# Optimization experiments

Measured on AMD Instinct MI355X. Metric: run time of the kernel, lower is better.

The kernel has to match this reference:

```python
import jax, jax.numpy as jnp
import numpy as np

HEAD_DIM = 128
N_HEADS = 16
N_KV_HEADS = 4
ROPE_BASE = 10000.0
TRAIN_SEQ_LEN = 1024


def _rotary_cos_sin(seq_len, rd, base=ROPE_BASE, train_len=TRAIN_SEQ_LEN):
    # NTK-style base scaling when seq_len exceeds training length (matches Rotary.forward)
    if seq_len > train_len:
        scale = seq_len / train_len
        base = base * scale ** (rd / (rd - 2))
    inv_freq = 1.0 / base ** (np.arange(0, rd, 2, dtype=np.float32) / rd)
    freqs = np.outer(np.arange(seq_len, dtype=np.float32), inv_freq)  # [T, rd/2]
    cos = jnp.asarray(np.cos(freqs))[None, :, None, :]  # [1,T,1,rd/2]
    sin = jnp.asarray(np.sin(freqs))[None, :, None, :]
    return cos, sin


def _apply_rotary(x, cos, sin):
    h = x.shape[-1] // 2
    x1, x2 = x[..., :h], x[..., h:]
    return jnp.concatenate((x1 * cos + x2 * sin, -x1 * sin + x2 * cos), axis=-1)


def _rms_norm(x):
    eps = jnp.finfo(x.dtype).eps
    return x * jax.lax.rsqrt(jnp.mean(x * x, axis=-1, keepdims=True) + eps)


def setup_inputs() -> dict:
    key = jax.random.key(0)
    ks = jax.random.split(key, 6)
    B, T, D = 4, 2048, 2048
    x = jax.random.normal(ks[0], (B, T, D), dtype=jnp.float32)
    q_w = jax.random.normal(ks[1], (D, D), dtype=jnp.float32) * 0.02
    k_w = jax.random.normal(ks[2], (N_KV_HEADS * HEAD_DIM, D), dtype=jnp.float32) * 0.02
    v_w = jax.random.normal(ks[3], (N_KV_HEADS * HEAD_DIM, D), dtype=jnp.float32) * 0.02
    out_w = jax.random.normal(ks[4], (D, D), dtype=jnp.float32) * 0.02
    q_gain = jnp.ones((N_HEADS,), dtype=jnp.float32)
    return {"x": x, "q_w": q_w, "k_w": k_w, "v_w": v_w, "out_w": out_w, "q_gain": q_gain}


def reference(x, q_w, k_w, v_w, out_w, q_gain):
    B, T, D = x.shape
    q = (x @ q_w.T).reshape(B, T, N_HEADS, HEAD_DIM)
    k = (x @ k_w.T).reshape(B, T, N_KV_HEADS, HEAD_DIM)
    v = (x @ v_w.T).reshape(B, T, N_KV_HEADS, HEAD_DIM)
    q = _rms_norm(q)
    k = _rms_norm(k)
    cos, sin = _rotary_cos_sin(T, HEAD_DIM)
    q = _apply_rotary(q, cos, sin)
    k = _apply_rotary(k, cos, sin)
    q = q * q_gain[None, None, :, None]
    # GQA: expand kv heads (repeat_interleave semantics)
    rep = N_HEADS // N_KV_HEADS
    k = jnp.repeat(k, rep, axis=2)  # [B,T,H,D]
    v = jnp.repeat(v, rep, axis=2)
    scale = 1.0 / jnp.sqrt(jnp.asarray(HEAD_DIM, dtype=x.dtype))
    scores = jnp.einsum("bthd,bshd->bhts", q, k) * scale  # [B,H,T,T]
    causal = jnp.tril(jnp.ones((T, T), dtype=bool))
    scores = jnp.where(causal[None, None], scores, jnp.asarray(-jnp.inf, dtype=scores.dtype))
    w = jax.nn.softmax(scores, axis=-1)
    y = jnp.einsum("bhts,bshd->bthd", w, v).reshape(B, T, D)
    return y @ out_w.T
```

## Files before the change

kernel.cpp:

```cpp
#include <hip/hip_runtime.h>
#include <hip/hip_bf16.h>
#include <math.h>

#define HEAD_DIM 128
#define NH 16
#define NKV 4
#define BB 4
#define TT 2048
#define DD 2048
#define ROWS (BB*TT)

typedef unsigned short u16;
typedef unsigned int u32;
typedef __attribute__((ext_vector_type(8))) short short8;
typedef __attribute__((ext_vector_type(4))) float f32x4;
typedef __attribute__((ext_vector_type(16))) float f32x16;
typedef __attribute__((ext_vector_type(4))) unsigned short u16x4;

__device__ __forceinline__ float bf2f(u16 u) {
    union { unsigned int i; float f; } v; v.i = ((unsigned int)u) << 16; return v.f;
}
__device__ __forceinline__ u16 f2bf(float f) {
    union { float f; unsigned int i; } v; v.f = f;
    unsigned int r = v.i + 0x7FFFu + ((v.i >> 16) & 1u);
    return (u16)(r >> 16);
}
__device__ __forceinline__ f32x4 mfma16(short8 a, short8 b, f32x4 c) {
    return __builtin_amdgcn_mfma_f32_16x16x32_bf16(a, b, c, 0, 0, 0);
}
__device__ __forceinline__ f32x16 mfma32(short8 a, short8 b, f32x16 c) {
    return __builtin_amdgcn_mfma_f32_32x32x16_bf16(a, b, c, 0, 0, 0);
}
__device__ __forceinline__ f32x16 zero16() {
    f32x16 z;
    #pragma unroll
    for (int i = 0; i < 16; ++i) z[i] = 0.f;
    return z;
}
__device__ __forceinline__ void gload_lds16(const u16* g, u16* l) {
    __builtin_amdgcn_global_load_lds(
        (const __attribute__((address_space(1))) unsigned int*)(const void*)g,
        (__attribute__((address_space(3))) unsigned int*)(void*)l, 16, 0, 0);
}

__global__ __launch_bounds__(256)
void cast_f2b(const float* __restrict__ in, u16* __restrict__ out, int n)
{
    int i = (blockIdx.x * 256 + threadIdx.x) * 4;
    if (i >= n) return;
    float4 v = *(const float4*)(in + i);
    u16x4 o;
    o.x = f2bf(v.x); o.y = f2bf(v.y); o.z = f2bf(v.z); o.w = f2bf(v.w);
    *(u16x4*)(out + i) = o;
}

__global__ __launch_bounds__(256)
void rope_table(float* __restrict__ cs, float* __restrict__ sn, float base)
{
    int idx = blockIdx.x * 256 + threadIdx.x;
    if (idx >= TT * 64) return;
    int t = idx >> 6;
    int d = idx & 63;
    float inv = powf(base, -(float)(2 * d) / 128.0f);
    float f = (float)t * inv;
    cs[idx] = cosf(f);
    sn[idx] = sinf(f);
}

__global__ __launch_bounds__(256)
void rmsrope_bf16(const u16* __restrict__ xin, u16* __restrict__ xout,
                  const float* __restrict__ cs, const float* __restrict__ sn,
                  const float* __restrict__ gain,
                  int heads, int use_gain, float pre, int relayout)
{
    int row  = blockIdx.x * 4 + (threadIdx.x >> 6);
    int lane = threadIdx.x & 63;
    int h = row % heads;
    int t = (row / heads) % TT;
    int b = row / (heads * TT);
    size_t base = (size_t)row * HEAD_DIM;

    float x1 = bf2f(xin[base + lane]);
    float x2 = bf2f(xin[base + 64 + lane]);
    float ss = x1 * x1 + x2 * x2;
    #pragma unroll
    for (int m = 1; m < 64; m <<= 1) ss += __shfl_xor(ss, m, 64);
    float r = 1.0f / sqrtf(ss * (1.0f / 128.0f) + 1.1920929e-7f);
    x1 *= r; x2 *= r;

    float c = cs[t * 64 + lane];
    float s = sn[t * 64 + lane];
    float o1 =  x1 * c + x2 * s;
    float o2 = -x1 * s + x2 * c;
    float g = use_gain ? gain[h] * pre : pre;
    o1 *= g; o2 *= g;

    size_t orow = relayout ? ((size_t)(b * heads + h) * TT + t) : (size_t)row;
    size_t obase = orow * HEAD_DIM;
    xout[obase + lane]      = f2bf(o1);
    xout[obase + 64 + lane] = f2bf(o2);
}

__global__ __launch_bounds__(256)
void transpose_v(const u16* __restrict__ vbh, u16* __restrict__ vtb)
{
    __shared__ u16 tile[64][72];
    const int tb = blockIdx.x;
    const int db = blockIdx.y;
    const int z  = blockIdx.z;
    const int tid = threadIdx.x;

    {
        const int r = tid >> 2, cq = tid & 3;
        const u16* src = vbh + ((size_t)(((z >> 2) * TT + tb * 64 + r) * NKV + (z & 3))) * 128
                             + db * 64 + cq * 16;
        short8 s0 = *(const short8*)(src);
        short8 s1 = *(const short8*)(src + 8);
        #pragma unroll
        for (int e = 0; e < 8; ++e) tile[r][cq * 16 + e]     = (u16)s0[e];
        #pragma unroll
        for (int e = 0; e < 8; ++e) tile[r][cq * 16 + 8 + e] = (u16)s1[e];
    }
    __syncthreads();
    {
        const int d = tid >> 2, tq = tid & 3;
        __attribute__((aligned(16))) u16 tmp[16];
        #pragma unroll
        for (int e = 0; e < 16; ++e) {
            int esw = (e & 3) | ((e & 4) << 1) | ((e & 8) >> 1);
            tmp[e] = tile[tq * 16 + esw][d];
        }
        u16* dst = vtb + (((size_t)(z * (TT / 64) + tb) * 128 + (db * 64 + d)) << 6) + tq * 16;
        *(short8*)(dst)     = ((short8*)tmp)[0];
        *(short8*)(dst + 8) = ((short8*)tmp)[1];
    }
}

template<int BN, int OUTMODE>
__global__ __launch_bounds__(512, 2)
void gemm256(const u16* __restrict__ A, const u16* __restrict__ W,
             void* __restrict__ C0, void* __restrict__ C1)
{
    constexpr int WN    = (BN == 256) ? 4 : 2;
    constexpr int MR    = (BN == 256) ? 8 : 4;
    constexpr int WROW  = (BN == 256) ? 128 : 64;
    constexpr int NT    = DD / 64;
    constexpr int BROWS = BN / 8;
    constexpr int NBI   = BROWS / 8;

    __shared__ u16 AsL[2 * 256 * 64];
    __shared__ u16 BsL[2 * BN * 64];

    const int tid = threadIdx.x;
    const int w = tid >> 6, l = tid & 63;
    const int lq = l & 15, lg = l >> 4;
    const int wmi = (WN == 4) ? (w >> 2) : (w >> 1);
    const int wni = w & (WN - 1);

    int bmi, bni;
    {
        const int bid = blockIdx.x;
        const int wg = (bid & 7) * 32 + (bid >> 3);
        const int st = wg >> 2, wi = wg & 3;
        const int sty = st >> 2, stx = st & 3;
        bmi = sty * 2 + (wi >> 1);
        bni = stx * 2 + (wi & 1);
    }
    const int bm = bmi * 256, bn = bni * BN;

    const int r8 = l >> 3;
    const int chs = (l & 7) ^ r8;
    const u16* Ag = A + (size_t)(bm + r8) * DD + chs * 8;
    const u16* Wg = W + (size_t)(bn + r8) * DD + chs * 8;

    f32x4 acc[MR][4];
    #pragma unroll
    for (int m = 0; m < MR; ++m)
        #pragma unroll
        for (int n = 0; n < 4; ++n) acc[m][n] = (f32x4){0.f, 0.f, 0.f, 0.f};

    auto stage = [&](int buf, int t) {
        const size_t ko = (size_t)t * 64;
        u16* Ad = AsL + buf * (256 * 64);
        u16* Bd = BsL + buf * (BN * 64);
        #pragma unroll
        for (int j = 0; j < 4; ++j) {
            int rb = w * 32 + j * 8;
            gload_lds16(Ag + (size_t)rb * DD + ko, Ad + rb * 64);
        }
        #pragma unroll
        for (int j = 0; j < NBI; ++j) {
            int rb = w * BROWS + j * 8;
            gload_lds16(Wg + (size_t)rb * DD + ko, Bd + rb * 64);
        }
    };

    stage(0, 0);
    stage(1, 1);
    if constexpr (BN == 256) asm volatile("s_waitcnt vmcnt(8)" ::: "memory");
    else                     asm volatile("s_waitcnt vmcnt(6)" ::: "memory");
    __builtin_amdgcn_s_barrier();
    __builtin_amdgcn_sched_barrier(0);

    const int swz = lq & 7;
    for (int t = 0; t < NT; ++t) {
        const int buf = t & 1;
        const u16* Ab = AsL + buf * (256 * 64);
        const u16* Bb = BsL + buf * (BN * 64);
        #pragma unroll
        for (int ks = 0; ks < 2; ++ks) {
            short8 af[MR], bf[4];
            #pragma unroll
            for (int m = 0; m < MR; ++m) {
                int arow = wmi * WROW + m * 16 + lq;
                af[m] = *(const short8*)(Ab + arow * 64 + (((ks * 4 + lg) ^ swz) << 3));
            }
            #pragma unroll
            for (int n = 0; n < 4; ++n) {
                int brow = wni * 64 + n * 16 + lq;
                bf[n] = *(const short8*)(Bb + brow * 64 + (((ks * 4 + lg) ^ swz) << 3));
            }
            __builtin_amdgcn_s_setprio(1);
            #pragma unroll
            for (int m = 0; m < MR; ++m)
                #pragma unroll
                for (int n = 0; n < 4; ++n)
                    acc[m][n] = mfma16(af[m], bf[n], acc[m][n]);
            __builtin_amdgcn_s_setprio(0);
        }

        if (t + 1 < NT) {
            __builtin_amdgcn_sched_barrier(0);
            __builtin_amdgcn_s_barrier();
            if (t + 2 < NT) {
                stage(buf, t + 2);
                if constexpr (BN == 256) asm volatile("s_waitcnt vmcnt(8)" ::: "memory");
                else                     asm volatile("s_waitcnt vmcnt(6)" ::: "memory");
            } else {
                asm volatile("s_waitcnt vmcnt(0)" ::: "memory");
            }
            __builtin_amdgcn_s_barrier();
            __builtin_amdgcn_sched_barrier(0);
        }
    }

    #pragma unroll
    for (int m = 0; m < MR; ++m) {
        int grow = bm + wmi * WROW + m * 16 + lg * 4;
        #pragma unroll
        for (int n = 0; n < 4; ++n) {
            int col = wni * 64 + n * 16 + lq;
            #pragma unroll
            for (int q = 0; q < 4; ++q) {
                float v = acc[m][n][q];
                if constexpr (OUTMODE == 0) {
                    ((u16*)C0)[(size_t)(grow + q) * 2048 + bn + col] = f2bf(v);
                } else if constexpr (OUTMODE == 2) {
                    ((float*)C0)[(size_t)(grow + q) * 2048 + bn + col] = v;
                } else {
                    int cg = bn + col;
                    if (cg < 512)
                        ((u16*)C0)[(size_t)(grow + q) * 512 + cg] = f2bf(v);
                    else
                        ((u16*)C1)[(size_t)(grow + q) * 512 + (cg - 512)] = f2bf(v);
                }
            }
        }
    }
}

__global__ __launch_bounds__(256, 2)
void attn_mfma(const u16* __restrict__ qg,
               const u16* __restrict__ kg,
               const u16* __restrict__ vtg,
               u16* __restrict__ yg)
{
    __shared__ u16 Ks[2][64 * 128];
    __shared__ u16 Vs[2][128 * 64];

    const int tid = threadIdx.x, wid = tid >> 6, l = tid & 63;
    const int lq = l & 31, hi = l >> 5, hi4 = hi << 2;

    const int bid = blockIdx.x;
    const int xcd  = bid & 7;
    const int s    = bid >> 3;
    const int gsub = s >> 5;
    const int hh   = (s >> 3) & 3;
    const int fold = s & 7;
    const int g    = xcd + (gsub << 3);
    const int b = g >> 2, kvh = g & 3;
    const int h = kvh * 4 + hh;

    const u16* kg_bh = kg + (((size_t)g * TT) << 7);
    const u16* vt_bh = vtg + (size_t)g * (TT / 64) * 8192;
    const u16* q_bh  = qg + (((size_t)(b * NH + h) * TT) << 7);

    const int nta = 2 * fold + 2;
    const int NT  = 34;

    const int krow = l >> 4;
    const int kch  = l & 15;
    const int vrow = l >> 3;
    const int vch  = l & 7;

    short8 sr[8];
    auto loadreg = [&](int kt) {
        const u16* ksrc = kg_bh + (((size_t)(kt * 64 + wid * 16)) << 7);
        const u16* vsrc = vt_bh + (size_t)kt * 8192 + wid * 2048;
        #pragma unroll
        for (int i = 0; i < 4; ++i) {
            sr[i]     = *(const short8*)(ksrc + (i * 4 + krow) * 128 + kch * 8);
            sr[4 + i] = *(const short8*)(vsrc + (i * 8 + vrow) * 64 + vch * 8);
        }
    };
    auto writelds = [&](int buf) {
        u16* kd = &Ks[buf][wid * 2048];
        u16* vd = &Vs[buf][wid * 2048];
        #pragma unroll
        for (int i = 0; i < 4; ++i) {
            int kr = i * 4 + krow;
            *(short8*)(kd + kr * 128 + ((kch ^ (kr & 7)) << 3)) = sr[i];
            int vr = i * 8 + vrow;
            *(short8*)(vd + vr * 64 + ((vch ^ (vr & 7)) << 3)) = sr[4 + i];
        }
    };

    loadreg(0);
    writelds(0);
    __syncthreads();

    int cur = 0, step = 0;

    for (int seg = 0; seg < 2; ++seg) {
        const int qblk = seg ? (15 - fold) : fold;
        const int nseg = seg ? (32 - 2 * fold) : nta;
        const int qrow = qblk * 128 + wid * 32 + lq;
        const int diag = (qblk * 128 + wid * 32) >> 6;

        const u16* qptr = q_bh + ((size_t)qrow << 7) + hi * 8;
        short8 qf[8];
        #pragma unroll
        for (int q = 0; q < 8; ++q)
            qf[q] = *(const short8*)(qptr + q * 16);

        f32x16 accO[4];
        #pragma unroll
        for (int d = 0; d < 4; ++d) accO[d] = zero16();
        float m2 = -1e30f, lr = 0.f;

        for (int kt = 0; kt < nseg; ++kt) {
            ++step;
            const bool more = step < NT;
            if (more) {
                int ktn = (step < nta) ? step : step - nta;
                loadreg(ktn);
            }

            if (kt <= diag) {
                const u16* Kc = Ks[cur];
                f32x16 accS0 = zero16(), accS1 = zero16();
                __builtin_amdgcn_s_setprio(1);
                #pragma unroll
                for (int ss = 0; ss < 8; ++ss) {
                    int c = ((2 * ss + hi) ^ (lq & 7)) << 3;
                    short8 kf0 = *(const short8*)(Kc + (lq << 7) + c);
                    accS0 = mfma32(kf0, qf[ss], accS0);
                    short8 kf1 = *(const short8*)(Kc + ((32 + lq) << 7) + c);
                    accS1 = mfma32(kf1, qf[ss], accS1);
                }
                __builtin_amdgcn_s_setprio(0);

                float p[32];
                if (kt == diag) {
                    #pragma unroll
                    for (int r = 0; r < 16; ++r) {
                        int key0 = kt * 64 + (r & 3) + 8 * (r >> 2) + hi4;
                        p[r]      = (key0      > qrow) ? -INFINITY : accS0[r];
                        p[16 + r] = (key0 + 32 > qrow) ? -INFINITY : accS1[r];
                    }
                } else {
                    #pragma unroll
                    for (int r = 0; r < 16; ++r) { p[r] = accS0[r]; p[16 + r] = accS1[r]; }
                }

                float t16[16];
                #pragma unroll
                for (int i = 0; i < 16; ++i) t16[i] = fmaxf(p[i], p[i + 16]);
                #pragma unroll
                for (int i = 0; i < 8; ++i) t16[i] = fmaxf(t16[i], t16[i + 8]);
                #pragma unroll
                for (int i = 0; i < 4; ++i) t16[i] = fmaxf(t16[i], t16[i + 4]);
                float pm = fmaxf(fmaxf(t16[0], t16[1]), fmaxf(t16[2], t16[3]));
                pm = fmaxf(pm, __shfl_xor(pm, 32, 64));

                float mn = m2;
                if (!__all(pm - m2 <= 8.0f)) {
                    mn = fmaxf(m2, pm);
                    float al = exp2f(m2 - mn);
                    lr *= al;
                    #pragma unroll
                    for (int d = 0; d < 4; ++d) accO[d] *= al;
                    m2 = mn;
                }

                #pragma unroll
                for (int r = 0; r < 32; ++r) p[r] = exp2f(p[r] - mn);
                #pragma unroll
                for (int i = 0; i < 16; ++i) t16[i] = p[i] + p[i + 16];
                #pragma unroll
                for (int i = 0; i < 8; ++i) t16[i] += t16[i + 8];
                #pragma unroll
                for (int i = 0; i < 4; ++i) t16[i] += t16[i + 4];
                float rs = (t16[0] + t16[1]) + (t16[2] + t16[3]);
                rs += __shfl_xor(rs, 32, 64);
                lr += rs;

                short8 pfrag[4];
                #pragma unroll
                for (int kb = 0; kb < 2; ++kb)
                    #pragma unroll
                    for (int c = 0; c < 2; ++c) {
                        union { u32 u[4]; short8 s8; } f;
                        #pragma unroll
                        for (int j = 0; j < 4; ++j) {
                            __hip_bfloat162 hb = __float22bfloat162_rn(
                                make_float2(p[kb * 16 + 8 * c + 2 * j],
                                            p[kb * 16 + 8 * c + 2 * j + 1]));
                            f.u[j] = *reinterpret_cast<u32*>(&hb);
                        }
                        pfrag[kb * 2 + c] = f.s8;
                    }

                const u16* Vc = Vs[cur];
                #pragma unroll
                for (int d = 0; d < 4; ++d) {
                    const u16* vr8 = Vc + ((d * 32 + lq) << 6);
                    short8 vf0 = *(const short8*)(vr8 + (((0 + hi) ^ (lq & 7)) << 3));
                    short8 vf1 = *(const short8*)(vr8 + (((2 + hi) ^ (lq & 7)) << 3));
                    short8 vf2 = *(const short8*)(vr8 + (((4 + hi) ^ (lq & 7)) << 3));
                    short8 vf3 = *(const short8*)(vr8 + (((6 + hi) ^ (lq & 7)) << 3));
                    __builtin_amdgcn_s_setprio(1);
                    accO[d] = mfma32(vf0, pfrag[0], accO[d]);
                    accO[d] = mfma32(vf1, pfrag[1], accO[d]);
                    accO[d] = mfma32(vf2, pfrag[2], accO[d]);
                    accO[d] = mfma32(vf3, pfrag[3], accO[d]);
                    __builtin_amdgcn_s_setprio(0);
                }
            }

            if (more) writelds(cur ^ 1);
            __syncthreads();
            cur ^= 1;
        }

        float inv = 1.0f / lr;
        u16* yrow = yg + ((size_t)((b * TT + qrow) * NH + h) << 7);
        #pragma unroll
        for (int d = 0; d < 4; ++d)
            #pragma unroll
            for (int r = 0; r < 4; ++r) {
                u16x4 o;
                #pragma unroll
                for (int q = 0; q < 4; ++q) o[q] = f2bf(accO[d][4 * r + q] * inv);
                *(u16x4*)(yrow + d * 32 + 8 * r + hi4) = o;
            }
    }
}

extern "C" void kernel_launch(void* const* d_in, const int* in_sizes, int n_in,
                              void* d_out, int out_size, void* d_ws, size_t ws_size,
                              hipStream_t stream)
{
    const float* x      = (const float*)d_in[0];
    const float* q_w    = (const float*)d_in[1];
    const float* k_w    = (const float*)d_in[2];
    const float* v_w    = (const float*)d_in[3];
    const float* out_w  = (const float*)d_in[4];
    const float* q_gain = (const float*)d_in[5];
    float* out = (float*)d_out;

    char* ws = (char*)d_ws;
    u16* qh   = (u16*)(ws);
    u16* xh   = (u16*)(ws + 33554432ull);
    u16* wqkv = (u16*)(ws + 67108864ull);
    u16* kh   = (u16*)(ws + 79691776ull);
    u16* vbh  = (u16*)(ws + 88080384ull);
    float* cs = (float*)(ws + 96468992ull);
    float* sn = cs + TT * 64;
    u16* wq   = wqkv;
    u16* wkv  = wqkv + 4194304;
    u16* q2   = xh;
    u16* kk   = wqkv;
    u16* vtb  = kh;
    u16* wout = vbh;
    u16* y    = qh;

    dim3 blk(256);

    double base = 10000.0 * pow((double)TT / 1024.0, 128.0 / 126.0);
    rope_table<<<(TT * 64) / 256, blk, 0, stream>>>(cs, sn, (float)base);

    cast_f2b<<<(ROWS * DD) / 1024, blk, 0, stream>>>(x, xh, ROWS * DD);
    cast_f2b<<<(DD * DD) / 1024, blk, 0, stream>>>(q_w, wq, DD * DD);
    cast_f2b<<<(512 * DD) / 1024, blk, 0, stream>>>(k_w, wkv, 512 * DD);
    cast_f2b<<<(512 * DD) / 1024, blk, 0, stream>>>(v_w, wkv + 1048576, 512 * DD);

    gemm256<256, 0><<<dim3(256), dim3(512), 0, stream>>>(xh, wq, qh, nullptr);
    gemm256<128, 1><<<dim3(256), dim3(512), 0, stream>>>(xh, wkv, kh, vbh);

    const float pre_q = 0.08838834764831845f * 1.4426950408889634f;
    rmsrope_bf16<<<(ROWS * NH) / 4, blk, 0, stream>>>(qh, q2, cs, sn, q_gain, NH, 1, pre_q, 1);
    rmsrope_bf16<<<(ROWS * NKV) / 4, blk, 0, stream>>>(kh, kk, cs, sn, nullptr, NKV, 0, 1.0f, 1);

    transpose_v<<<dim3(TT / 64, 2, BB * NKV), blk, 0, stream>>>(vbh, vtb);

    cast_f2b<<<(DD * DD) / 1024, blk, 0, stream>>>(out_w, wout, DD * DD);

    attn_mfma<<<dim3(512), blk, 0, stream>>>(q2, kk, vtb, y);

    gemm256<256, 2><<<dim3(256), dim3(512), 0, stream>>>(y, wout, out, nullptr);
}
```

Before: 355.0 us.

## Stage K/V tiles with direct global-to-LDS loads and two-tile prefetch

```diff
diff --git a/kernel.cpp b/kernel.cpp
--- a/kernel.cpp
+++ b/kernel.cpp
@@ -298,38 +298,30 @@
     const int nta = 2 * fold + 2;
     const int NT  = 34;
 
-    const int krow = l >> 4;
-    const int kch  = l & 15;
-    const int vrow = l >> 3;
-    const int vch  = l & 7;
-
-    short8 sr[8];
-    auto loadreg = [&](int kt) {
-        const u16* ksrc = kg_bh + (((size_t)(kt * 64 + wid * 16)) << 7);
-        const u16* vsrc = vt_bh + (size_t)kt * 8192 + wid * 2048;
+    const int kro = l >> 4;
+    const int kch = l & 15;
+    const int vro = l >> 3;
+    const int vchs = (l & 7) ^ vro;
+
+    auto stage = [&](int buf, int kt) {
         #pragma unroll
         for (int i = 0; i < 4; ++i) {
-            sr[i]     = *(const short8*)(ksrc + (i * 4 + krow) * 128 + kch * 8);
-            sr[4 + i] = *(const short8*)(vsrc + (i * 8 + vrow) * 64 + vch * 8);
+            int kr = wid * 16 + i * 4 + kro;
+            gload_lds16(kg_bh + (((size_t)(kt * 64 + kr)) << 7) + ((kch ^ (kr & 7)) << 3),
+                        &Ks[buf][(wid * 16 + i * 4) << 7]);
+            int vr = wid * 32 + i * 8 + vro;
+            gload_lds16(vt_bh + (size_t)kt * 8192 + (vr << 6) + (vchs << 3),
+                        &Vs[buf][(wid * 32 + i * 8) << 6]);
         }
     };
-    auto writelds = [&](int buf) {
-        u16* kd = &Ks[buf][wid * 2048];
-        u16* vd = &Vs[buf][wid * 2048];
-        #pragma unroll
-        for (int i = 0; i < 4; ++i) {
-            int kr = i * 4 + krow;
-            *(short8*)(kd + kr * 128 + ((kch ^ (kr & 7)) << 3)) = sr[i];
-            int vr = i * 8 + vrow;
-            *(short8*)(vd + vr * 64 + ((vch ^ (vr & 7)) << 3)) = sr[4 + i];
-        }
-    };
-
-    loadreg(0);
-    writelds(0);
-    __syncthreads();
-
-    int cur = 0, step = 0;
+
+    stage(0, 0);
+    stage(1, 1);
+    asm volatile("s_waitcnt vmcnt(8)" ::: "memory");
+    __builtin_amdgcn_s_barrier();
+    __builtin_amdgcn_sched_barrier(0);
+
+    int step = 0;
 
     for (int seg = 0; seg < 2; ++seg) {
         const int qblk = seg ? (15 - fold) : fold;
@@ -348,16 +340,11 @@
         for (int d = 0; d < 4; ++d) accO[d] = zero16();
         float m2 = -1e30f, lr = 0.f;
 
-        for (int kt = 0; kt < nseg; ++kt) {
-            ++step;
-            const bool more = step < NT;
-            if (more) {
-                int ktn = (step < nta) ? step : step - nta;
-                loadreg(ktn);
-            }
+        for (int kt = 0; kt < nseg; ++kt, ++step) {
+            const int buf = step & 1;
 
             if (kt <= diag) {
-                const u16* Kc = Ks[cur];
+                const u16* Kc = Ks[buf];
                 f32x16 accS0 = zero16(), accS1 = zero16();
                 __builtin_amdgcn_s_setprio(1);
                 #pragma unroll
@@ -431,7 +418,7 @@
                         pfrag[kb * 2 + c] = f.s8;
                     }
 
-                const u16* Vc = Vs[cur];
+                const u16* Vc = Vs[buf];
                 #pragma unroll
                 for (int d = 0; d < 4; ++d) {
                     const u16* vr8 = Vc + ((d * 32 + lq) << 6);
@@ -448,9 +435,19 @@
                 }
             }
 
-            if (more) writelds(cur ^ 1);
-            __syncthreads();
-            cur ^= 1;
+            if (step + 1 < NT) {
+                __builtin_amdgcn_sched_barrier(0);
+                __builtin_amdgcn_s_barrier();
+                if (step + 2 < NT) {
+                    int tn = step + 2;
+                    stage(buf, (tn < nta) ? tn : tn - nta);
+                    asm volatile("s_waitcnt vmcnt(8)" ::: "memory");
+                } else {
+                    asm volatile("s_waitcnt vmcnt(0)" ::: "memory");
+                }
+                __builtin_amdgcn_s_barrier();
+                __builtin_amdgcn_sched_barrier(0);
+            }
         }
 
         float inv = 1.0f / lr;
```

Result: no change. 354.8 us (-0.1%).
